# Performance work log

Measured on AMD Instinct MI355X. Metric: run time of the kernel, lower is better.

The kernel has to match this reference:

```python
import jax, jax.numpy as jnp
import numpy as np

N = 500_000
K = 16
E = N * K
H = 256


def _linear_params(key, fan_in, fan_out):
    k1, k2 = jax.random.split(key)
    bound = 1.0 / np.sqrt(fan_in)
    W = jax.random.uniform(k1, (fan_in, fan_out), jnp.float32, -bound, bound)
    b = jax.random.uniform(k2, (fan_out,), jnp.float32, -bound, bound)
    return W, b


def setup_inputs() -> dict:
    key = jax.random.key(0)
    ks = jax.random.split(key, 10)
    x = jax.random.normal(ks[0], (N, 3), jnp.float32)
    edge_index = jax.random.randint(ks[1], (2, E), 0, N, jnp.int64)
    edge_attr = jax.random.normal(ks[2], (E, 1), jnp.float32)
    W1, b1 = _linear_params(ks[3], K, H)          # GNN1 message MLP: Linear(k, 256)
    We1, be1 = _linear_params(ks[4], H, 128)      # encoder Linear(256,128)
    We2, be2 = _linear_params(ks[5], 128, 6)      # encoder Linear(128,6)
    Wd1, bd1 = _linear_params(ks[6], 6, 128)      # decoder Linear(6,128)
    Wd2, bd2 = _linear_params(ks[7], 128, H)      # decoder Linear(128,256)
    Wo, bo = _linear_params(ks[8], H, 1)          # output Linear(256,1)
    return {"x": x, "edge_index": edge_index, "edge_attr": edge_attr,
            "W1": W1, "b1": b1, "We1": We1, "be1": be1, "We2": We2, "be2": be2,
            "Wd1": Wd1, "bd1": bd1, "Wd2": Wd2, "bd2": bd2, "Wo": Wo, "bo": bo}


def reference(x, edge_index, edge_attr, W1, b1, We1, be1, We2, be2,
              Wd1, bd1, Wd2, bd2, Wo, bo):
    # GNN1: messages are edge_attr verbatim (x_i/x_j ignored); aggregate reshapes
    # all E scalar messages into (N, k) (k edges per node, contiguous) and runs
    # Linear(k,256)+Tanh. Note: LSTM and GCN4 branches in the torch code are dead
    # (GNN1 ignores its node-feature input), so they do not affect the output.
    k = W1.shape[0]
    msgs = edge_attr.reshape(-1, k)                    # (N, k)
    h = jnp.tanh(msgs @ W1 + b1)                       # (N, 256)
    # second L1 call produces the identical result (depends only on edge_attr)
    z = jnp.tanh(jnp.tanh(h @ We1 + be1) @ We2 + be2)  # encoder -> (N, 6)
    d = jnp.tanh(z @ Wd1 + bd1) @ Wd2 + bd2            # decoder -> (N, 256)
    out = jax.nn.sigmoid(jnp.tanh(d) @ Wo + bo)        # (N, 1)
    return out[:, 0]                                   # squeeze(dim=1) -> (N,)
```

## Files before the change

kernel.cpp:

```cpp
#include <hip/hip_runtime.h>


#define N_NODES 500000

#define OFF_W1 0
#define OFF_W2 8192
#define OFF_W3 73728
#define OFF_W4 77824
#define OFF_W5 86016
#define OFF_WO 151552
#define OFF_B1 152576
#define OFF_B2 153600
#define OFF_B3 154112
#define OFF_B4 154176
#define OFF_B5 154688
#define OFF_EXTRA 155712
#define OFF_ZERO  155728
#define IMG_END   156240
#define IMG_ALLOC 156672

#define LDS_SZ IMG_ALLOC

#define SCONST (-2.8853900817779268f)

typedef _Float16 half8  __attribute__((ext_vector_type(8)));
typedef __fp16   pk16x2 __attribute__((ext_vector_type(2)));
typedef float    f32x4  __attribute__((ext_vector_type(4)));
typedef int      int4v  __attribute__((ext_vector_type(4)));

__device__ __align__(16) char g_img[IMG_ALLOC];

static __device__ __forceinline__ unsigned pack_f16_rne(float a, float b) {
  _Float16 ha = (_Float16)a, hb = (_Float16)b;
  unsigned short ua = __builtin_bit_cast(unsigned short, ha);
  unsigned short ub = __builtin_bit_cast(unsigned short, hb);
  return (unsigned)ua | ((unsigned)ub << 16);
}
static __device__ __forceinline__ int pkrtz(float a, float b) {
  pk16x2 h = __builtin_amdgcn_cvt_pkrtz(a, b);
  return __builtin_bit_cast(int, h);
}
static __device__ __forceinline__ float sig2(float y) {
  float e = __builtin_amdgcn_exp2f(y);
  return __builtin_amdgcn_rcpf(1.0f + e);
}
static __device__ __forceinline__ float sigmoid_f(float x) {
  float e = __builtin_amdgcn_exp2f(x * -1.4426950408889634f);
  return __builtin_amdgcn_rcpf(1.0f + e);
}
static __device__ __forceinline__ f32x4 mfma16(half8 a, int4v b, f32x4 c) {
  return __builtin_amdgcn_mfma_f32_16x16x32_f16(a, __builtin_bit_cast(half8, b), c, 0, 0, 0);
}
static __device__ __forceinline__ half8 lda(const char* smem, int off) {
  return *(const half8*)(smem + off);
}
static __device__ __forceinline__ f32x4 ldf4(const char* smem, int off) {
  return *(const f32x4*)(smem + off);
}
#define FENCE() __builtin_amdgcn_sched_barrier(0)

struct PK2 { int lo, hi; };
static __device__ __forceinline__ PK2 tp(f32x4 a) {
  PK2 p;
  p.lo = pkrtz(sig2(a.x), sig2(a.y));
  p.hi = pkrtz(sig2(a.z), sig2(a.w));
  return p;
}

__global__ void gnn_prep(const float* __restrict__ W1,  const float* __restrict__ b1,
                         const float* __restrict__ We1, const float* __restrict__ be1,
                         const float* __restrict__ We2, const float* __restrict__ be2,
                         const float* __restrict__ Wd1, const float* __restrict__ bd1,
                         const float* __restrict__ Wd2, const float* __restrict__ bd2,
                         const float* __restrict__ Wo,  const float* __restrict__ bo)
{
  int t = blockIdx.x * 256 + threadIdx.x;
  int off = t * 4;
  if (off >= IMG_END) return;
  unsigned val;
  if (off < OFF_W2) {
    int rel = off;
    int mi = rel >> 9, li = (rel >> 4) & 31, j2 = (rel >> 2) & 3;
    int fout = mi * 16 + (li & 15);
    int k0 = (li >> 4) * 8 + j2 * 2;
    val = pack_f16_rne(SCONST * W1[k0 * 256 + fout], SCONST * W1[(k0 + 1) * 256 + fout]);
  } else if (off < OFF_W3) {
    int rel = off - OFF_W2;
    int blk = rel >> 10, li = (rel >> 4) & 63, j2 = (rel >> 2) & 3;
    int mi = blk >> 3, ki = blk & 7;
    int fout = mi * 16 + (li & 15);
    int k0 = ki * 32 + 4 * (li >> 4) + 16 * (j2 >> 1) + 2 * (j2 & 1);
    val = pack_f16_rne(2.0f * SCONST * We1[k0 * 128 + fout],
                       2.0f * SCONST * We1[(k0 + 1) * 128 + fout]);
  } else if (off < OFF_W4) {
    int rel = off - OFF_W3;
    int ki = rel >> 10, li = (rel >> 4) & 63, j2 = (rel >> 2) & 3;
    int fo = li & 15;
    int k0 = ki * 32 + 4 * (li >> 4) + 16 * (j2 >> 1) + 2 * (j2 & 1);
    float a = (fo < 6) ? 2.0f * SCONST * We2[k0 * 6 + fo] : 0.0f;
    float b = (fo < 6) ? 2.0f * SCONST * We2[(k0 + 1) * 6 + fo] : 0.0f;
    val = pack_f16_rne(a, b);
  } else if (off < OFF_W5) {
    int rel = off - OFF_W4;
    int mi = rel >> 10, li = (rel >> 4) & 63, j2 = (rel >> 2) & 3;
    int fout = mi * 16 + (li & 15);
    int qa = li >> 4;
    unsigned v = 0;
    if (j2 < 2) {
      int k0 = 4 * qa + 2 * j2;
      float a = (k0 < 6)     ? 2.0f * SCONST * Wd1[k0 * 128 + fout]       : 0.0f;
      float b = (k0 + 1 < 6) ? 2.0f * SCONST * Wd1[(k0 + 1) * 128 + fout] : 0.0f;
      v = pack_f16_rne(a, b);
    }
    val = v;
  } else if (off < OFF_WO) {
    int rel = off - OFF_W5;
    int blk = rel >> 10, li = (rel >> 4) & 63, j2 = (rel >> 2) & 3;
    int mi = blk >> 2, ki = blk & 3;
    int fout = mi * 16 + (li & 15);
    int k0 = ki * 32 + 4 * (li >> 4) + 16 * (j2 >> 1) + 2 * (j2 & 1);
    val = pack_f16_rne(2.0f * SCONST * Wd2[k0 * 256 + fout],
                       2.0f * SCONST * Wd2[(k0 + 1) * 256 + fout]);
  } else if (off < OFF_B1) {
    val = __builtin_bit_cast(unsigned, 2.0f * Wo[(off - OFF_WO) >> 2]);
  } else if (off < OFF_B2) {
    val = __builtin_bit_cast(unsigned, SCONST * b1[(off - OFF_B1) >> 2]);
  } else if (off < OFF_B3) {
    int i = (off - OFF_B2) >> 2;
    float s = 0.0f;
    for (int k = 0; k < 256; ++k) s += We1[k * 128 + i];
    val = __builtin_bit_cast(unsigned, SCONST * (be1[i] - s));
  } else if (off < OFF_B4) {
    int i = (off - OFF_B3) >> 2;
    float v = 0.0f;
    if (i < 6) {
      float s = 0.0f;
      for (int k = 0; k < 128; ++k) s += We2[k * 6 + i];
      v = SCONST * (be2[i] - s);
    }
    val = __builtin_bit_cast(unsigned, v);
  } else if (off < OFF_B5) {
    int i = (off - OFF_B4) >> 2;
    float s = 0.0f;
    for (int k = 0; k < 6; ++k) s += Wd1[k * 128 + i];
    val = __builtin_bit_cast(unsigned, SCONST * (bd1[i] - s));
  } else if (off < OFF_EXTRA) {
    int i = (off - OFF_B5) >> 2;
    float s = 0.0f;
    for (int k = 0; k < 128; ++k) s += Wd2[k * 256 + i];
    val = __builtin_bit_cast(unsigned, SCONST * (bd2[i] - s));
  } else if (off == OFF_EXTRA) {
    float s = 0.0f;
    for (int k = 0; k < 256; ++k) s += Wo[k];
    val = __builtin_bit_cast(unsigned, bo[0] - s);
  } else {
    val = 0;
  }
  *(unsigned*)(g_img + off) = val;
}

static __device__ __forceinline__ void stage_chunk(const char* src, char* dst) {
  __builtin_amdgcn_global_load_lds(
      (const __attribute__((address_space(1))) void*)src,
      (__attribute__((address_space(3))) void*)dst, 16, 0, 0);
}

#define L1_PAIR(KO, OUT_G0, OUT_G1) do {                                   \
    half8 Ae = lda(smem, w1b + (2*(KO))*w1s);                              \
    half8 Ao = lda(smem, w1b + (2*(KO)+1)*w1s);                            \
    f32x4 be_ = ldf4(smem, OFF_B1 + (2*(KO))*64 + q*16);                   \
    f32x4 bo_ = ldf4(smem, OFF_B1 + (2*(KO)+1)*64 + q*16);                 \
    f32x4 ae0 = mfma16(Ae, b1g0, be_);                                     \
    f32x4 ae1 = mfma16(Ae, b1g1, be_);                                     \
    f32x4 ao0 = mfma16(Ao, b1g0, bo_);                                     \
    f32x4 ao1 = mfma16(Ao, b1g1, bo_);                                     \
    PK2 pe0 = tp(ae0), po0 = tp(ao0), pe1 = tp(ae1), po1 = tp(ao1);        \
    OUT_G0.x = pe0.lo; OUT_G0.y = pe0.hi; OUT_G0.z = po0.lo; OUT_G0.w = po0.hi; \
    OUT_G1.x = pe1.lo; OUT_G1.y = pe1.hi; OUT_G1.z = po1.lo; OUT_G1.w = po1.hi; \
    FENCE();                                                               \
  } while (0)

#define L2_MI(MI, ACC0, ACC1) do {                                                            \
    f32x4 bb = ldf4(smem, OFF_B2 + (MI)*64 + q*16);                                           \
    ACC0 = bb; ACC1 = bb;                                                                     \
    half8 A;                                                                                  \
    A = lda(smem, OFF_W2 + ((MI)*8+0)*1024 + ln*16); ACC0 = mfma16(A, c2g0_0, ACC0); ACC1 = mfma16(A, c2g1_0, ACC1); \
    A = lda(smem, OFF_W2 + ((MI)*8+1)*1024 + ln*16); ACC0 = mfma16(A, c2g0_1, ACC0); ACC1 = mfma16(A, c2g1_1, ACC1); \
    A = lda(smem, OFF_W2 + ((MI)*8+2)*1024 + ln*16); ACC0 = mfma16(A, c2g0_2, ACC0); ACC1 = mfma16(A, c2g1_2, ACC1); \
    A = lda(smem, OFF_W2 + ((MI)*8+3)*1024 + ln*16); ACC0 = mfma16(A, c2g0_3, ACC0); ACC1 = mfma16(A, c2g1_3, ACC1); \
    A = lda(smem, OFF_W2 + ((MI)*8+4)*1024 + ln*16); ACC0 = mfma16(A, c2g0_4, ACC0); ACC1 = mfma16(A, c2g1_4, ACC1); \
    A = lda(smem, OFF_W2 + ((MI)*8+5)*1024 + ln*16); ACC0 = mfma16(A, c2g0_5, ACC0); ACC1 = mfma16(A, c2g1_5, ACC1); \
    A = lda(smem, OFF_W2 + ((MI)*8+6)*1024 + ln*16); ACC0 = mfma16(A, c2g0_6, ACC0); ACC1 = mfma16(A, c2g1_6, ACC1); \
    A = lda(smem, OFF_W2 + ((MI)*8+7)*1024 + ln*16); ACC0 = mfma16(A, c2g0_7, ACC0); ACC1 = mfma16(A, c2g1_7, ACC1); \
  } while (0)

#define L2_PAIR(KO, OUT_G0, OUT_G1) do {                                   \
    f32x4 ve0, ve1, vo0, vo1;                                              \
    L2_MI(2*(KO),   ve0, ve1);                                             \
    FENCE();                                                               \
    L2_MI(2*(KO)+1, vo0, vo1);                                             \
    PK2 pe0 = tp(ve0), po0 = tp(vo0), pe1 = tp(ve1), po1 = tp(vo1);        \
    OUT_G0.x = pe0.lo; OUT_G0.y = pe0.hi; OUT_G0.z = po0.lo; OUT_G0.w = po0.hi; \
    OUT_G1.x = pe1.lo; OUT_G1.y = pe1.hi; OUT_G1.z = po1.lo; OUT_G1.w = po1.hi; \
    FENCE();                                                               \
  } while (0)

#define L4_MI(MI, ACC0, ACC1) do {                                         \
    f32x4 bb = ldf4(smem, OFF_B4 + (MI)*64 + q*16);                        \
    half8 A = lda(smem, OFF_W4 + (MI)*1024 + ln*16);                       \
    ACC0 = mfma16(A, b4g0, bb);                                            \
    ACC1 = mfma16(A, b4g1, bb);                                            \
  } while (0)

#define L4_PAIR(KO, OUT_G0, OUT_G1) do {                                   \
    f32x4 ve0, ve1, vo0, vo1;                                              \
    L4_MI(2*(KO),   ve0, ve1);                                             \
    L4_MI(2*(KO)+1, vo0, vo1);                                             \
    PK2 pe0 = tp(ve0), po0 = tp(vo0), pe1 = tp(ve1), po1 = tp(vo1);        \
    OUT_G0.x = pe0.lo; OUT_G0.y = pe0.hi; OUT_G0.z = po0.lo; OUT_G0.w = po0.hi; \
    OUT_G1.x = pe1.lo; OUT_G1.y = pe1.hi; OUT_G1.z = po1.lo; OUT_G1.w = po1.hi; \
    FENCE();                                                               \
  } while (0)

#define L5_MI(MI) do {                                                                        \
    f32x4 bb = ldf4(smem, OFF_B5 + (MI)*64 + q*16);                                           \
    f32x4 a0 = bb, a1 = bb;                                                                   \
    half8 A;                                                                                  \
    A = lda(smem, OFF_W5 + ((MI)*4+0)*1024 + ln*16); a0 = mfma16(A, c5g0_0, a0); a1 = mfma16(A, c5g1_0, a1); \
    A = lda(smem, OFF_W5 + ((MI)*4+1)*1024 + ln*16); a0 = mfma16(A, c5g0_1, a0); a1 = mfma16(A, c5g1_1, a1); \
    A = lda(smem, OFF_W5 + ((MI)*4+2)*1024 + ln*16); a0 = mfma16(A, c5g0_2, a0); a1 = mfma16(A, c5g1_2, a1); \
    A = lda(smem, OFF_W5 + ((MI)*4+3)*1024 + ln*16); a0 = mfma16(A, c5g0_3, a0); a1 = mfma16(A, c5g1_3, a1); \
    f32x4 wo = ldf4(smem, OFF_WO + (MI)*64 + q*16);                                           \
    part0 += sig2(a0.x)*wo.x + sig2(a0.y)*wo.y + sig2(a0.z)*wo.z + sig2(a0.w)*wo.w;           \
    part1 += sig2(a1.x)*wo.x + sig2(a1.y)*wo.y + sig2(a1.z)*wo.z + sig2(a1.w)*wo.w;           \
    FENCE();                                                                                  \
  } while (0)

__global__ __launch_bounds__(512)
void gnn_fused(const float* __restrict__ ea, float* __restrict__ out)
{
  __shared__ __align__(16) char smem[LDS_SZ];
  const int tid = threadIdx.x;
  const int wv = tid >> 6, ln = tid & 63;

#pragma unroll 1
  for (int r = 0; r < 20; ++r) {
    int cb = (r * 8 + wv) << 6;
    if (cb < 9765) {
      stage_chunk(g_img + (size_t)cb * 16 + ln * 16,
                  smem + (size_t)cb * 16 + ln * 16);
    }
  }
  __syncthreads();

  const int q = ln >> 4, c = ln & 15;
  const bool qlo = (q < 2);
  const int lnl16 = (ln & 31) * 16;
  const int w1b = qlo ? (OFF_W1 + lnl16) : (OFF_ZERO + lnl16);
  const int w1s = qlo ? 512 : 0;
  const float bo2 = *(const float*)(smem + OFF_EXTRA);

  const int NG = N_NODES / 32;
  const int g0i = blockIdx.x * 8 + wv;
  const int gstep = gridDim.x << 3;
#pragma unroll 1
  for (int g = g0i; g < NG; g += gstep) {
    const int base = g * 32;

    int nl = base + (q >> 1) * 16 + c;
    if (nl > N_NODES - 1) nl = N_NODES - 1;
    const f32x4* ea4 = (const f32x4*)ea;
    size_t eb = (size_t)nl * 4 + (size_t)((q & 1) * 2);
    f32x4 vlo = ea4[eb];
    f32x4 vhi = ea4[eb + 1];
    int4v b1g0;
    b1g0.x = pkrtz(vlo.x, vlo.y); b1g0.y = pkrtz(vlo.z, vlo.w);
    b1g0.z = pkrtz(vhi.x, vhi.y); b1g0.w = pkrtz(vhi.z, vhi.w);
    int sh = (ln + 32) & 63;
    int4v b1g1;
    b1g1.x = __shfl(b1g0.x, sh, 64); b1g1.y = __shfl(b1g0.y, sh, 64);
    b1g1.z = __shfl(b1g0.z, sh, 64); b1g1.w = __shfl(b1g0.w, sh, 64);

    int4v c2g0_0, c2g0_1, c2g0_2, c2g0_3, c2g0_4, c2g0_5, c2g0_6, c2g0_7;
    int4v c2g1_0, c2g1_1, c2g1_2, c2g1_3, c2g1_4, c2g1_5, c2g1_6, c2g1_7;
    L1_PAIR(0, c2g0_0, c2g1_0);
    L1_PAIR(1, c2g0_1, c2g1_1);
    L1_PAIR(2, c2g0_2, c2g1_2);
    L1_PAIR(3, c2g0_3, c2g1_3);
    L1_PAIR(4, c2g0_4, c2g1_4);
    L1_PAIR(5, c2g0_5, c2g1_5);
    L1_PAIR(6, c2g0_6, c2g1_6);
    L1_PAIR(7, c2g0_7, c2g1_7);

    int4v c3g0_0, c3g0_1, c3g0_2, c3g0_3;
    int4v c3g1_0, c3g1_1, c3g1_2, c3g1_3;
    L2_PAIR(0, c3g0_0, c3g1_0);
    L2_PAIR(1, c3g0_1, c3g1_1);
    L2_PAIR(2, c3g0_2, c3g1_2);
    L2_PAIR(3, c3g0_3, c3g1_3);

    f32x4 bb3 = ldf4(smem, OFF_B3 + q * 16);
    f32x4 z0 = bb3, z1 = bb3;
    half8 A;
    A = lda(smem, OFF_W3 + 0 * 1024 + ln * 16); z0 = mfma16(A, c3g0_0, z0); z1 = mfma16(A, c3g1_0, z1);
    A = lda(smem, OFF_W3 + 1 * 1024 + ln * 16); z0 = mfma16(A, c3g0_1, z0); z1 = mfma16(A, c3g1_1, z1);
    A = lda(smem, OFF_W3 + 2 * 1024 + ln * 16); z0 = mfma16(A, c3g0_2, z0); z1 = mfma16(A, c3g1_2, z1);
    A = lda(smem, OFF_W3 + 3 * 1024 + ln * 16); z0 = mfma16(A, c3g0_3, z0); z1 = mfma16(A, c3g1_3, z1);
    PK2 p3g0 = tp(z0);
    PK2 p3g1 = tp(z1);
    FENCE();

    int4v b4g0, b4g1;
    b4g0.x = p3g0.lo; b4g0.y = p3g0.hi; b4g0.z = 0; b4g0.w = 0;
    b4g1.x = p3g1.lo; b4g1.y = p3g1.hi; b4g1.z = 0; b4g1.w = 0;

    int4v c5g0_0, c5g0_1, c5g0_2, c5g0_3;
    int4v c5g1_0, c5g1_1, c5g1_2, c5g1_3;
    L4_PAIR(0, c5g0_0, c5g1_0);
    L4_PAIR(1, c5g0_1, c5g1_1);
    L4_PAIR(2, c5g0_2, c5g1_2);
    L4_PAIR(3, c5g0_3, c5g1_3);

    float part0 = 0.0f, part1 = 0.0f;
    L5_MI(0);  L5_MI(1);  L5_MI(2);  L5_MI(3);
    L5_MI(4);  L5_MI(5);  L5_MI(6);  L5_MI(7);
    L5_MI(8);  L5_MI(9);  L5_MI(10); L5_MI(11);
    L5_MI(12); L5_MI(13); L5_MI(14); L5_MI(15);

    part0 += __shfl_xor(part0, 16, 64); part0 += __shfl_xor(part0, 32, 64);
    part1 += __shfl_xor(part1, 16, 64); part1 += __shfl_xor(part1, 32, 64);
    if (q < 2) {
      int node = base + q * 16 + c;
      if (node < N_NODES) {
        float v = ((q == 0) ? part0 : part1) + bo2;
        out[node] = sigmoid_f(v);
      }
    }
  }
}

extern "C" void kernel_launch(void* const* d_in, const int* in_sizes, int n_in,
                              void* d_out, int out_size, void* d_ws, size_t ws_size,
                              hipStream_t stream) {
  (void)in_sizes; (void)n_in; (void)ws_size; (void)out_size; (void)d_ws;
  const float* ea  = (const float*)d_in[2];
  const float* W1  = (const float*)d_in[3];
  const float* b1  = (const float*)d_in[4];
  const float* We1 = (const float*)d_in[5];
  const float* be1 = (const float*)d_in[6];
  const float* We2 = (const float*)d_in[7];
  const float* be2 = (const float*)d_in[8];
  const float* Wd1 = (const float*)d_in[9];
  const float* bd1 = (const float*)d_in[10];
  const float* Wd2 = (const float*)d_in[11];
  const float* bd2 = (const float*)d_in[12];
  const float* Wo  = (const float*)d_in[13];
  const float* bo  = (const float*)d_in[14];

  gnn_prep<<<dim3((IMG_END / 4 + 255) / 256), dim3(256), 0, stream>>>(
      W1, b1, We1, be1, We2, be2, Wd1, bd1, Wd2, bd2, Wo, bo);
  gnn_fused<<<dim3(256), dim3(512), 0, stream>>>(ea, (float*)d_out);
}
```

Baseline: 242.9 us.

## Split bias folding into a parallel prep kernel and drop scheduling fences

After: 238.8 us. About the same (-1.7%).

```diff
diff --git a/kernel.cpp b/kernel.cpp
--- a/kernel.cpp
+++ b/kernel.cpp
@@ -67,16 +67,78 @@
   return p;
 }
 
+__global__ __launch_bounds__(1024)
+void gnn_prep_bias(const float* __restrict__ We1, const float* __restrict__ be1,
+                   const float* __restrict__ We2, const float* __restrict__ be2,
+                   const float* __restrict__ Wd1, const float* __restrict__ bd1,
+                   const float* __restrict__ Wd2, const float* __restrict__ bd2,
+                   const float* __restrict__ Wo,  const float* __restrict__ bo)
+{
+  __shared__ float sb[2048];
+  const int t = threadIdx.x;
+
+  if (t < 512) {
+    int col = t & 127, part = t >> 7;
+    float s = 0.0f;
+    for (int r = 0; r < 64; ++r) s += We1[(part * 64 + r) * 128 + col];
+    sb[t] = s;
+  } else {
+    int u = t - 512;
+    int col = u & 255, part = u >> 8;
+    float s = 0.0f;
+    for (int r = 0; r < 64; ++r) s += Wd2[(part * 64 + r) * 256 + col];
+    sb[512 + u] = s;
+  }
+  __syncthreads();
+
+  if (t < 768)             sb[1024 + t] = We2[t];
+  else if (t < 1024)       sb[1792 + (t - 768)] = Wo[t - 768];
+  __syncthreads();
+
+  float* gB2 = (float*)(g_img + OFF_B2);
+  float* gB3 = (float*)(g_img + OFF_B3);
+  float* gB4 = (float*)(g_img + OFF_B4);
+  float* gB5 = (float*)(g_img + OFF_B5);
+
+  if (t < 128) {
+    float s = sb[t] + sb[128 + t] + sb[256 + t] + sb[384 + t];
+    gB2[t] = SCONST * (be1[t] - s);
+  } else if (t < 384) {
+    int col = t - 128;
+    float s = sb[512 + col] + sb[768 + col];
+    gB5[col] = SCONST * (bd2[col] - s);
+  } else if (t < 400) {
+    int i = t - 384;
+    if (i < 6) {
+      float s = 0.0f;
+      for (int k = 0; k < 128; ++k) s += sb[1024 + k * 6 + i];
+      gB3[i] = SCONST * (be2[i] - s);
+    } else {
+      gB3[i] = 0.0f;
+    }
+  } else if (t == 400) {
+    float s = 0.0f;
+    for (int k = 0; k < 256; ++k) s += sb[1792 + k];
+    *(float*)(g_img + OFF_EXTRA) = bo[0] - s;
+  } else if (t >= 401 && t < 529) {
+    int i = t - 401;
+    float s = 0.0f;
+    for (int k = 0; k < 6; ++k) s += Wd1[k * 128 + i];
+    gB4[i] = SCONST * (bd1[i] - s);
+  }
+}
+
 __global__ void gnn_prep(const float* __restrict__ W1,  const float* __restrict__ b1,
-                         const float* __restrict__ We1, const float* __restrict__ be1,
-                         const float* __restrict__ We2, const float* __restrict__ be2,
-                         const float* __restrict__ Wd1, const float* __restrict__ bd1,
-                         const float* __restrict__ Wd2, const float* __restrict__ bd2,
-                         const float* __restrict__ Wo,  const float* __restrict__ bo)
+                         const float* __restrict__ We1,
+                         const float* __restrict__ We2,
+                         const float* __restrict__ Wd1,
+                         const float* __restrict__ Wd2,
+                         const float* __restrict__ Wo)
 {
   int t = blockIdx.x * 256 + threadIdx.x;
   int off = t * 4;
   if (off >= IMG_END) return;
+  if (off >= OFF_B2 && off < OFF_EXTRA + 4) return;
   unsigned val;
   if (off < OFF_W2) {
     int rel = off;
@@ -125,34 +187,6 @@
     val = __builtin_bit_cast(unsigned, 2.0f * Wo[(off - OFF_WO) >> 2]);
   } else if (off < OFF_B2) {
     val = __builtin_bit_cast(unsigned, SCONST * b1[(off - OFF_B1) >> 2]);
-  } else if (off < OFF_B3) {
-    int i = (off - OFF_B2) >> 2;
-    float s = 0.0f;
-    for (int k = 0; k < 256; ++k) s += We1[k * 128 + i];
-    val = __builtin_bit_cast(unsigned, SCONST * (be1[i] - s));
-  } else if (off < OFF_B4) {
-    int i = (off - OFF_B3) >> 2;
-    float v = 0.0f;
-    if (i < 6) {
-      float s = 0.0f;
-      for (int k = 0; k < 128; ++k) s += We2[k * 6 + i];
-      v = SCONST * (be2[i] - s);
-    }
-    val = __builtin_bit_cast(unsigned, v);
-  } else if (off < OFF_B5) {
-    int i = (off - OFF_B4) >> 2;
-    float s = 0.0f;
-    for (int k = 0; k < 6; ++k) s += Wd1[k * 128 + i];
-    val = __builtin_bit_cast(unsigned, SCONST * (bd1[i] - s));
-  } else if (off < OFF_EXTRA) {
-    int i = (off - OFF_B5) >> 2;
-    float s = 0.0f;
-    for (int k = 0; k < 128; ++k) s += Wd2[k * 256 + i];
-    val = __builtin_bit_cast(unsigned, SCONST * (bd2[i] - s));
-  } else if (off == OFF_EXTRA) {
-    float s = 0.0f;
-    for (int k = 0; k < 256; ++k) s += Wo[k];
-    val = __builtin_bit_cast(unsigned, bo[0] - s);
   } else {
     val = 0;
   }
@@ -219,7 +253,6 @@
     PK2 pe0 = tp(ve0), po0 = tp(vo0), pe1 = tp(ve1), po1 = tp(vo1);        \
     OUT_G0.x = pe0.lo; OUT_G0.y = pe0.hi; OUT_G0.z = po0.lo; OUT_G0.w = po0.hi; \
     OUT_G1.x = pe1.lo; OUT_G1.y = pe1.hi; OUT_G1.z = po1.lo; OUT_G1.w = po1.hi; \
-    FENCE();                                                               \
   } while (0)
 
 #define L5_MI(MI) do {                                                                        \
@@ -233,7 +266,6 @@
     f32x4 wo = ldf4(smem, OFF_WO + (MI)*64 + q*16);                                           \
     part0 += sig2(a0.x)*wo.x + sig2(a0.y)*wo.y + sig2(a0.z)*wo.z + sig2(a0.w)*wo.w;           \
     part1 += sig2(a1.x)*wo.x + sig2(a1.y)*wo.y + sig2(a1.z)*wo.z + sig2(a1.w)*wo.w;           \
-    FENCE();                                                                                  \
   } while (0)
 
 __global__ __launch_bounds__(512)
@@ -268,7 +300,6 @@
     const int base = g * 32;
 
     int nl = base + (q >> 1) * 16 + c;
-    if (nl > N_NODES - 1) nl = N_NODES - 1;
     const f32x4* ea4 = (const f32x4*)ea;
     size_t eb = (size_t)nl * 4 + (size_t)((q & 1) * 2);
     f32x4 vlo = ea4[eb];
@@ -331,10 +362,8 @@
     part1 += __shfl_xor(part1, 16, 64); part1 += __shfl_xor(part1, 32, 64);
     if (q < 2) {
       int node = base + q * 16 + c;
-      if (node < N_NODES) {
-        float v = ((q == 0) ? part0 : part1) + bo2;
-        out[node] = sigmoid_f(v);
-      }
+      float v = ((q == 0) ? part0 : part1) + bo2;
+      out[node] = sigmoid_f(v);
     }
   }
 }
@@ -357,7 +386,9 @@
   const float* Wo  = (const float*)d_in[13];
   const float* bo  = (const float*)d_in[14];
 
+  gnn_prep_bias<<<dim3(1), dim3(1024), 0, stream>>>(
+      We1, be1, We2, be2, Wd1, bd1, Wd2, bd2, Wo, bo);
   gnn_prep<<<dim3((IMG_END / 4 + 255) / 256), dim3(256), 0, stream>>>(
-      W1, b1, We1, be1, We2, be2, Wd1, bd1, Wd2, bd2, Wo, bo);
+      W1, b1, We1, We2, Wd1, Wd2, Wo);
   gnn_fused<<<dim3(256), dim3(512), 0, stream>>>(ea, (float*)d_out);
 }
```
